# Kernel optimization log

Hardware: AMD Instinct MI355X
Metric: run time of the kernel (lower is better)

The kernel has to match this reference:

```python
import jax, jax.numpy as jnp
import numpy as np

H = 64
VOCAB = 128
LN_EPS = 1e-5
NORM_EPS = 1e-12


def _l2norm(k):
    # F.normalize(..., dim=-1): x / max(||x||_2, eps)
    n = jnp.sqrt(jnp.sum(k * k, axis=-1, keepdims=True))
    return k / jnp.maximum(n, NORM_EPS)


def _delta_scan(M0, ks, vs):
    # ks, vs: [L, B, H] time-major; M0: [B, H, H]
    def step(M, kv):
        k, v = kv
        Mk = jnp.einsum('bij,bj->bi', M, k)            # [B,H]
        M = M + (v - Mk)[:, :, None] * k[:, None, :]   # rank-1 update
        return M, None
    M, _ = jax.lax.scan(step, M0, (ks, vs))
    return M


def reference(x, embed, W1, b1, W2, b2, ln_g, ln_b, Wk, Wv, Wq, Wattn, Wout, bout):
    # Encoder: embed -> residual FF -> LayerNorm
    h = embed[x]                                        # [B,L,H]
    ff = jnp.maximum(h @ W1.T + b1, 0.0) @ W2.T + b2
    z = h + ff
    mu = jnp.mean(z, axis=-1, keepdims=True)
    var = jnp.mean((z - mu) ** 2, axis=-1, keepdims=True)
    hidden = (z - mu) / jnp.sqrt(var + LN_EPS) * ln_g + ln_b  # [B,L,H]

    B, L, _ = hidden.shape
    # First delta-rule memory write over all L steps
    ks = _l2norm(hidden @ Wk.T)                         # [B,L,H]
    vs = hidden @ Wv.T                                  # [B,L,H]
    M0 = jnp.zeros((B, H, H), dtype=hidden.dtype)
    M = _delta_scan(M0, jnp.swapaxes(ks, 0, 1), jnp.swapaxes(vs, 0, 1))

    half = L // 2
    slots = jnp.swapaxes(M, 1, 2)                       # [B,H,H] = M^T
    q = hidden[:, :half, :] @ Wattn.T                   # [B,half,H]
    # bmm(q, slots^T) = q @ M
    attn = jax.nn.softmax(jnp.einsum('bth,bhk->btk', q, M) / jnp.sqrt(jnp.asarray(H, hidden.dtype)), axis=-1)
    ctx = jnp.einsum('btk,bkh->bth', attn, slots)       # [B,half,H]

    # Second delta-rule write seeded from M
    ks2 = _l2norm(ctx @ Wk.T)
    vs2 = ctx @ Wv.T
    M2 = _delta_scan(M, jnp.swapaxes(ks2, 0, 1), jnp.swapaxes(vs2, 0, 1))

    q_last = hidden[:, -1, :] @ Wq.T                    # [B,H]
    read = jnp.einsum('bij,bj->bi', M2, q_last)         # [B,H]
    return read @ Wout.T + bout                         # [B,VOCAB]


def setup_inputs() -> dict:
    key = jax.random.key(0)
    ks = jax.random.split(key, 16)
    B, L = 64, 4096
    s = 0.05
    return {
        'x': jax.random.randint(ks[0], (B, L), 0, VOCAB),
        'embed': jax.random.normal(ks[1], (VOCAB, H), jnp.float32) * s,
        'W1': jax.random.normal(ks[2], (2 * H, H), jnp.float32) * s,
        'b1': jnp.zeros((2 * H,), jnp.float32),
        'W2': jax.random.normal(ks[3], (H, 2 * H), jnp.float32) * s,
        'b2': jnp.zeros((H,), jnp.float32),
        'ln_g': jnp.ones((H,), jnp.float32),
        'ln_b': jnp.zeros((H,), jnp.float32),
        'Wk': jax.random.normal(ks[4], (H, H), jnp.float32) * s,
        'Wv': jax.random.normal(ks[5], (H, H), jnp.float32) * s,
        'Wq': jax.random.normal(ks[6], (H, H), jnp.float32) * s,
        'Wattn': jax.random.normal(ks[7], (H, H), jnp.float32) * s,
        'Wout': jax.random.normal(ks[8], (VOCAB, H), jnp.float32) * s,
        'bout': jnp.zeros((VOCAB,), jnp.float32),
    }
```

## Files before the change

### kernel.cpp

```cpp
#include <hip/hip_runtime.h>

#define SEQL 4096
#define NB 64

__device__ __forceinline__ float dpp_xor1_add(float x) {
    int v = __builtin_amdgcn_mov_dpp(__float_as_int(x), 0xB1, 0xF, 0xF, true);
    return x + __int_as_float(v);
}
__device__ __forceinline__ float dpp_xor2_add(float x) {
    int v = __builtin_amdgcn_mov_dpp(__float_as_int(x), 0x4E, 0xF, 0xF, true);
    return x + __int_as_float(v);
}

#define FMA16(A, W, H)                                      \
    A[0]  = fmaf(W.x, H.x, A[0]);  A[1]  = fmaf(W.x, H.y, A[1]);   \
    A[2]  = fmaf(W.x, H.z, A[2]);  A[3]  = fmaf(W.x, H.w, A[3]);   \
    A[4]  = fmaf(W.y, H.x, A[4]);  A[5]  = fmaf(W.y, H.y, A[5]);   \
    A[6]  = fmaf(W.y, H.z, A[6]);  A[7]  = fmaf(W.y, H.w, A[7]);   \
    A[8]  = fmaf(W.z, H.x, A[8]);  A[9]  = fmaf(W.z, H.y, A[9]);   \
    A[10] = fmaf(W.z, H.z, A[10]); A[11] = fmaf(W.z, H.w, A[11]);  \
    A[12] = fmaf(W.w, H.x, A[12]); A[13] = fmaf(W.w, H.y, A[13]);  \
    A[14] = fmaf(W.w, H.z, A[14]); A[15] = fmaf(W.w, H.w, A[15])

__device__ __forceinline__ void proj_tile64(const float* __restrict__ sW,
                                            const float* __restrict__ sA,
                                            int jq, int tq, float* __restrict__ a)
{
#pragma unroll
    for (int u = 0; u < 16; ++u) a[u] = 0.f;
#pragma unroll 4
    for (int i = 0; i < 64; ++i) {
        float4 w  = *reinterpret_cast<const float4*>(&sW[i * 68 + jq]);
        float4 h4 = *reinterpret_cast<const float4*>(&sA[i * 68 + tq]);
        FMA16(a, w, h4);
    }
}

__device__ __forceinline__ void load_w_t(const float* __restrict__ W, int ldw, int col0,
                                         int tid, float4* __restrict__ r)
{
    const int j = tid & 63;
    const int cq0 = tid >> 6;
#pragma unroll
    for (int it = 0; it < 4; ++it)
        r[it] = *reinterpret_cast<const float4*>(&W[(size_t)j * ldw + col0 + (it * 4 + cq0) * 4]);
}
__device__ __forceinline__ void write_w_t(const float4* __restrict__ r,
                                          float* __restrict__ sWb, int tid)
{
    const int j = tid & 63;
    const int cq0 = tid >> 6;
#pragma unroll
    for (int it = 0; it < 4; ++it) {
        const int c = (it * 4 + cq0) * 4;
        sWb[(c + 0) * 68 + j] = r[it].x;
        sWb[(c + 1) * 68 + j] = r[it].y;
        sWb[(c + 2) * 68 + j] = r[it].z;
        sWb[(c + 3) * 68 + j] = r[it].w;
    }
}

__device__ __forceinline__ void stage_w_t(const float* __restrict__ W, int ldw, int col0,
                                          float* __restrict__ sWb, int tid)
{
    float4 r[4];
    load_w_t(W, ldw, col0, tid, r);
    write_w_t(r, sWb, tid);
}
__device__ __forceinline__ void stage_w_n(const float* __restrict__ W,
                                          float* __restrict__ sWb, int tid)
{
#pragma unroll
    for (int it = 0; it < 4; ++it) {
        int item = it * 256 + tid;
        int r = item >> 4, c4 = item & 15;
        float4 w = *reinterpret_cast<const float4*>(&W[(size_t)r * 64 + c4 * 4]);
        *reinterpret_cast<float4*>(&sWb[r * 68 + c4 * 4]) = w;
    }
}

__global__ __launch_bounds__(256) void encoder_kernel(
    const int* __restrict__ x, const float* __restrict__ embed,
    const float* __restrict__ W1, const float* __restrict__ b1,
    const float* __restrict__ W2, const float* __restrict__ b2,
    const float* __restrict__ ln_g, const float* __restrict__ ln_b,
    const float* __restrict__ Wk, const float* __restrict__ Wv,
    const float* __restrict__ Wq,
    float* __restrict__ ks, float* __restrict__ vs,
    float* __restrict__ hidT, float* __restrict__ qlast)
{
    __shared__ __align__(16) float sZ[64 * 68];
    __shared__ __align__(16) float sF[64 * 68];
    __shared__ __align__(16) float sW[64 * 68];

    const int tid = threadIdx.x;
    const size_t g0 = (size_t)blockIdx.x * 64;
    const int b = (int)(g0 >> 12);
    const int l0 = (int)(g0 & (SEQL - 1));
    const int jq = (tid & 15) * 4;
    const int tq = (tid >> 4) * 4;
    const bool doq = (l0 < 2048);
    const bool dolast = (l0 == SEQL - 64);

    float4 pf[4], pf2[4];

    load_w_t(W1, 64, 0, tid, pf);
    for (int idx = tid; idx < 4096; idx += 256) {
        int t = idx >> 6, i = idx & 63;
        sZ[i * 68 + t] = embed[(size_t)x[g0 + t] * 64 + i];
    }
    write_w_t(pf, sW, tid);
    load_w_t(W2, 128, 0, tid, pf2);
    __syncthreads();

    float zacc[16];
#pragma unroll
    for (int u = 0; u < 16; ++u) zacc[u] = 0.f;

    {
        float a[16];
        proj_tile64(sW, sZ, jq, tq, a);
        float4 bb = *reinterpret_cast<const float4*>(&b1[jq]);
        float bv[4] = {bb.x, bb.y, bb.z, bb.w};
#pragma unroll
        for (int u = 0; u < 4; ++u) {
            float4 o;
            o.x = fmaxf(a[u * 4 + 0] + bv[u], 0.f);
            o.y = fmaxf(a[u * 4 + 1] + bv[u], 0.f);
            o.z = fmaxf(a[u * 4 + 2] + bv[u], 0.f);
            o.w = fmaxf(a[u * 4 + 3] + bv[u], 0.f);
            *reinterpret_cast<float4*>(&sF[(jq + u) * 68 + tq]) = o;
        }
    }
    __syncthreads();
    write_w_t(pf2, sW, tid);
    load_w_t(W1 + 4096, 64, 0, tid, pf);
    __syncthreads();
#pragma unroll 4
    for (int p = 0; p < 64; ++p) {
        float4 w  = *reinterpret_cast<const float4*>(&sW[p * 68 + jq]);
        float4 f4 = *reinterpret_cast<const float4*>(&sF[p * 68 + tq]);
        FMA16(zacc, w, f4);
    }
    __syncthreads();
    write_w_t(pf, sW, tid);
    load_w_t(W2, 128, 64, tid, pf2);
    __syncthreads();
    {
        float a[16];
        proj_tile64(sW, sZ, jq, tq, a);
        float4 bb = *reinterpret_cast<const float4*>(&b1[64 + jq]);
        float bv[4] = {bb.x, bb.y, bb.z, bb.w};
#pragma unroll
        for (int u = 0; u < 4; ++u) {
            float4 o;
            o.x = fmaxf(a[u * 4 + 0] + bv[u], 0.f);
            o.y = fmaxf(a[u * 4 + 1] + bv[u], 0.f);
            o.z = fmaxf(a[u * 4 + 2] + bv[u], 0.f);
            o.w = fmaxf(a[u * 4 + 3] + bv[u], 0.f);
            *reinterpret_cast<float4*>(&sF[(jq + u) * 68 + tq]) = o;
        }
    }
    __syncthreads();
    write_w_t(pf2, sW, tid);
    load_w_t(Wk, 64, 0, tid, pf);
    load_w_t(Wv, 64, 0, tid, pf2);
    __syncthreads();
#pragma unroll 4
    for (int p = 0; p < 64; ++p) {
        float4 w  = *reinterpret_cast<const float4*>(&sW[p * 68 + jq]);
        float4 f4 = *reinterpret_cast<const float4*>(&sF[p * 68 + tq]);
        FMA16(zacc, w, f4);
    }

    {
        float z[16];
        float4 b2v = *reinterpret_cast<const float4*>(&b2[jq]);
        float bv[4] = {b2v.x, b2v.y, b2v.z, b2v.w};
#pragma unroll
        for (int u = 0; u < 4; ++u) {
            float4 h4 = *reinterpret_cast<const float4*>(&sZ[(jq + u) * 68 + tq]);
            z[u * 4 + 0] = h4.x + bv[u] + zacc[u * 4 + 0];
            z[u * 4 + 1] = h4.y + bv[u] + zacc[u * 4 + 1];
            z[u * 4 + 2] = h4.z + bv[u] + zacc[u * 4 + 2];
            z[u * 4 + 3] = h4.w + bv[u] + zacc[u * 4 + 3];
        }
        float s[4], ss[4];
#pragma unroll
        for (int v = 0; v < 4; ++v) {
            s[v]  = z[v] + z[4 + v] + z[8 + v] + z[12 + v];
            ss[v] = z[v] * z[v] + z[4 + v] * z[4 + v]
                  + z[8 + v] * z[8 + v] + z[12 + v] * z[12 + v];
        }
#pragma unroll
        for (int m = 1; m <= 8; m <<= 1) {
#pragma unroll
            for (int v = 0; v < 4; ++v) {
                s[v]  += __shfl_xor(s[v], m);
                ss[v] += __shfl_xor(ss[v], m);
            }
        }
        float mu[4], inv[4];
#pragma unroll
        for (int v = 0; v < 4; ++v) {
            mu[v] = s[v] * 0.015625f;
            float var = ss[v] * 0.015625f - mu[v] * mu[v];
            inv[v] = rsqrtf(var + 1e-5f);
        }
        float4 g4  = *reinterpret_cast<const float4*>(&ln_g[jq]);
        float4 be4 = *reinterpret_cast<const float4*>(&ln_b[jq]);
        float gv[4] = {g4.x, g4.y, g4.z, g4.w};
        float bev[4] = {be4.x, be4.y, be4.z, be4.w};
#pragma unroll
        for (int u = 0; u < 4; ++u) {
            float4 o;
            o.x = (z[u * 4 + 0] - mu[0]) * inv[0] * gv[u] + bev[u];
            o.y = (z[u * 4 + 1] - mu[1]) * inv[1] * gv[u] + bev[u];
            o.z = (z[u * 4 + 2] - mu[2]) * inv[2] * gv[u] + bev[u];
            o.w = (z[u * 4 + 3] - mu[3]) * inv[3] * gv[u] + bev[u];
            *reinterpret_cast<float4*>(&sZ[(jq + u) * 68 + tq]) = o;
        }
    }
    __syncthreads();
    write_w_t(pf, sW, tid);
    write_w_t(pf2, sF, tid);
    if (dolast) load_w_t(Wq, 64, 0, tid, pf);
    __syncthreads();

    {
        float a[16];
        proj_tile64(sW, sZ, jq, tq, a);
        float ssq[4];
#pragma unroll
        for (int v = 0; v < 4; ++v)
            ssq[v] = a[v] * a[v] + a[4 + v] * a[4 + v]
                   + a[8 + v] * a[8 + v] + a[12 + v] * a[12 + v];
#pragma unroll
        for (int m = 1; m <= 8; m <<= 1) {
#pragma unroll
            for (int v = 0; v < 4; ++v) ssq[v] += __shfl_xor(ssq[v], m);
        }
#pragma unroll
        for (int v = 0; v < 4; ++v) {
            float sc = 1.f / fmaxf(sqrtf(ssq[v]), 1e-12f);
            float4 o = make_float4(a[v] * sc, a[4 + v] * sc, a[8 + v] * sc, a[12 + v] * sc);
            *reinterpret_cast<float4*>(&ks[(g0 + tq + v) * 64 + jq]) = o;
        }
    }
    {
        float a[16];
        proj_tile64(sF, sZ, jq, tq, a);
#pragma unroll
        for (int v = 0; v < 4; ++v) {
            float4 o = make_float4(a[v], a[4 + v], a[8 + v], a[12 + v]);
            *reinterpret_cast<float4*>(&vs[(g0 + tq + v) * 64 + jq]) = o;
        }
    }

    if (doq) {
#pragma unroll
        for (int it = 0; it < 4; ++it) {
            int item = it * 256 + tid;
            int i = item >> 4, q4 = (item & 15) * 4;
            float4 v = *reinterpret_cast<const float4*>(&sZ[i * 68 + q4]);
            *reinterpret_cast<float4*>(&hidT[((size_t)b * 64 + i) * 2048 + l0 + q4]) = v;
        }
    }

    if (dolast) {
        __syncthreads();
        write_w_t(pf, sW, tid);
        __syncthreads();
        float a[16];
        proj_tile64(sW, sZ, jq, tq, a);
        if ((tid >> 4) == 15) {
            float4 o = make_float4(a[3], a[7], a[11], a[15]);
            *reinterpret_cast<float4*>(&qlast[(size_t)b * 64 + jq]) = o;
        }
    }
}

__global__ __launch_bounds__(256) void precompute_kernel(
    const float* __restrict__ Mbuf, const float* __restrict__ Wattn,
    const float* __restrict__ Wk, const float* __restrict__ Wv,
    float* __restrict__ WAM, float* __restrict__ MK, float* __restrict__ MV)
{
    __shared__ __align__(16) float sM[64 * 68];
    __shared__ __align__(16) float sOp[64 * 68];
    const int b = blockIdx.x;
    const int tid = threadIdx.x;
    const int jq = (tid & 15) * 4;
    const int tq = (tid >> 4) * 4;
    const float* Mb = Mbuf + (size_t)b * 4096;

    stage_w_n(Mb, sM, tid);
    stage_w_n(Wattn, sOp, tid);
    __syncthreads();
    {
        float a[16];
        proj_tile64(sM, sOp, jq, tq, a);
#pragma unroll
        for (int v = 0; v < 4; ++v)
            *reinterpret_cast<float4*>(&WAM[(size_t)b * 4096 + (tq + v) * 64 + jq]) =
                make_float4(a[v], a[4 + v], a[8 + v], a[12 + v]);
    }
    __syncthreads();
    stage_w_t(Wk, 64, 0, sOp, tid);
    __syncthreads();
    {
        float a[16];
        proj_tile64(sM, sOp, jq, tq, a);
#pragma unroll
        for (int v = 0; v < 4; ++v)
            *reinterpret_cast<float4*>(&MK[(size_t)b * 4096 + (tq + v) * 64 + jq]) =
                make_float4(a[v], a[4 + v], a[8 + v], a[12 + v]);
    }
    __syncthreads();
    stage_w_t(Wv, 64, 0, sOp, tid);
    __syncthreads();
    {
        float a[16];
        proj_tile64(sM, sOp, jq, tq, a);
#pragma unroll
        for (int v = 0; v < 4; ++v)
            *reinterpret_cast<float4*>(&MV[(size_t)b * 4096 + (tq + v) * 64 + jq]) =
                make_float4(a[v], a[4 + v], a[8 + v], a[12 + v]);
    }
}

#define STEP2(K0, K1, K2, K3, V)                                                \
    do {                                                                        \
        float dp0 = fmaf(p[0], K0.x, fmaf(p[1], K0.y, fmaf(p[2], K0.z, p[3] * K0.w))); \
        float dp1 = fmaf(p[4], K1.x, fmaf(p[5], K1.y, fmaf(p[6], K1.z, p[7] * K1.w))); \
        float dp2 = fmaf(p[8], K2.x, fmaf(p[9], K2.y, fmaf(p[10], K2.z, p[11] * K2.w))); \
        float dp3 = fmaf(p[12], K3.x, fmaf(p[13], K3.y, fmaf(p[14], K3.z, p[15] * K3.w))); \
        float dq0 = fmaf(q[0], K0.x, fmaf(q[1], K0.y, fmaf(q[2], K0.z, q[3] * K0.w))); \
        float dq1 = fmaf(q[4], K1.x, fmaf(q[5], K1.y, fmaf(q[6], K1.z, q[7] * K1.w))); \
        float dq2 = fmaf(q[8], K2.x, fmaf(q[9], K2.y, fmaf(q[10], K2.z, q[11] * K2.w))); \
        float dq3 = fmaf(q[12], K3.x, fmaf(q[13], K3.y, fmaf(q[14], K3.z, q[15] * K3.w))); \
        float ddp = (dp0 + dp1) + (dp2 + dp3);                                  \
        float ddq = (dq0 + dq1) + (dq2 + dq3);                                  \
        ddp = dpp_xor1_add(ddp);  ddq = dpp_xor1_add(ddq);                      \
        ddp = dpp_xor2_add(ddp);  ddq = dpp_xor2_add(ddq);                      \
        float up = -ddp;                                                        \
        float uq = V - ddq;                                                     \
        p[0] = fmaf(up, K0.x, p[0]);   q[0] = fmaf(uq, K0.x, q[0]);             \
        p[1] = fmaf(up, K0.y, p[1]);   q[1] = fmaf(uq, K0.y, q[1]);             \
        p[2] = fmaf(up, K0.z, p[2]);   q[2] = fmaf(uq, K0.z, q[2]);             \
        p[3] = fmaf(up, K0.w, p[3]);   q[3] = fmaf(uq, K0.w, q[3]);             \
        p[4] = fmaf(up, K1.x, p[4]);   q[4] = fmaf(uq, K1.x, q[4]);             \
        p[5] = fmaf(up, K1.y, p[5]);   q[5] = fmaf(uq, K1.y, q[5]);             \
        p[6] = fmaf(up, K1.z, p[6]);   q[6] = fmaf(uq, K1.z, q[6]);             \
        p[7] = fmaf(up, K1.w, p[7]);   q[7] = fmaf(uq, K1.w, q[7]);             \
        p[8] = fmaf(up, K2.x, p[8]);   q[8] = fmaf(uq, K2.x, q[8]);             \
        p[9] = fmaf(up, K2.y, p[9]);   q[9] = fmaf(uq, K2.y, q[9]);             \
        p[10] = fmaf(up, K2.z, p[10]); q[10] = fmaf(uq, K2.z, q[10]);           \
        p[11] = fmaf(up, K2.w, p[11]); q[11] = fmaf(uq, K2.w, q[11]);           \
        p[12] = fmaf(up, K3.x, p[12]); q[12] = fmaf(uq, K3.x, q[12]);           \
        p[13] = fmaf(up, K3.y, p[13]); q[13] = fmaf(uq, K3.y, q[13]);           \
        p[14] = fmaf(up, K3.z, p[14]); q[14] = fmaf(uq, K3.z, q[14]);           \
        p[15] = fmaf(up, K3.w, p[15]); q[15] = fmaf(uq, K3.w, q[15]);           \
    } while (0)

__global__ __launch_bounds__(256) void chunk_kernel(
    float* __restrict__ ksb, float* __restrict__ vsb, int C)
{
    __shared__ __align__(16) float sk[2][32 * 64];
    __shared__ __align__(16) float sv[2][32 * 64];

    const int job = blockIdx.x;
    const int tid = threadIdx.x;
    const int r = tid >> 2;
    const int c0 = (tid & 3) * 16;
    float* kc = ksb + (size_t)job * C * 64;
    float* vc = vsb + (size_t)job * C * 64;

    float p[16], q[16];
#pragma unroll
    for (int j = 0; j < 16; ++j) { p[j] = (c0 + j == r) ? 1.f : 0.f; q[j] = 0.f; }

    const int nt = C >> 5;
    float4 rk0, rk1, rv0, rv1;

    {
        const float4* gk = reinterpret_cast<const float4*>(kc);
        const float4* gv = reinterpret_cast<const float4*>(vc);
        float4 a0 = gk[tid], a1 = gk[256 + tid];
        float4 b0 = gv[tid], b1 = gv[256 + tid];
        float4* dk = reinterpret_cast<float4*>(sk[0]);
        float4* dv = reinterpret_cast<float4*>(sv[0]);
        dk[tid] = a0; dk[256 + tid] = a1;
        dv[tid] = b0; dv[256 + tid] = b1;
    }
    if (nt > 1) {
        const float4* gk = reinterpret_cast<const float4*>(kc + 2048);
        const float4* gv = reinterpret_cast<const float4*>(vc + 2048);
        rk0 = gk[tid]; rk1 = gk[256 + tid];
        rv0 = gv[tid]; rv1 = gv[256 + tid];
    }
    __syncthreads();

    int cur = 0;
    for (int tile = 0; tile < nt; ++tile) {
        if (tile + 1 < nt) {
            float4* dk = reinterpret_cast<float4*>(sk[cur ^ 1]);
            float4* dv = reinterpret_cast<float4*>(sv[cur ^ 1]);
            dk[tid] = rk0; dk[256 + tid] = rk1;
            dv[tid] = rv0; dv[256 + tid] = rv1;
            if (tile + 2 < nt) {
                const float4* gk = reinterpret_cast<const float4*>(kc + (size_t)(tile + 2) * 2048);
                const float4* gv = reinterpret_cast<const float4*>(vc + (size_t)(tile + 2) * 2048);
                rk0 = gk[tid]; rk1 = gk[256 + tid];
                rv0 = gv[tid]; rv1 = gv[256 + tid];
            }
        }

        const float* kl = sk[cur] + c0;
        const float* vl = sv[cur] + r;
        float4 a0, a1, a2, a3, e0, e1, e2, e3;
        float va, ve;
        {
            const float4* kp = reinterpret_cast<const float4*>(kl);
            a0 = kp[0]; a1 = kp[1]; a2 = kp[2]; a3 = kp[3];
            va = vl[0];
        }
#pragma unroll
        for (int t = 0; t < 32; t += 2) {
            {
                const float4* kp = reinterpret_cast<const float4*>(kl + (t + 1) * 64);
                e0 = kp[0]; e1 = kp[1]; e2 = kp[2]; e3 = kp[3];
                ve = vl[(t + 1) * 64];
            }
            STEP2(a0, a1, a2, a3, va);
            if (t + 2 < 32) {
                const float4* kp = reinterpret_cast<const float4*>(kl + (t + 2) * 64);
                a0 = kp[0]; a1 = kp[1]; a2 = kp[2]; a3 = kp[3];
                va = vl[(t + 2) * 64];
            }
            STEP2(e0, e1, e2, e3, ve);
        }
        __syncthreads();
        cur ^= 1;
    }

    float4* po = reinterpret_cast<float4*>(kc + r * 64 + c0);
    po[0] = make_float4(p[0], p[1], p[2], p[3]);
    po[1] = make_float4(p[4], p[5], p[6], p[7]);
    po[2] = make_float4(p[8], p[9], p[10], p[11]);
    po[3] = make_float4(p[12], p[13], p[14], p[15]);
    float4* qo = reinterpret_cast<float4*>(vc + r * 64 + c0);
    qo[0] = make_float4(q[0], q[1], q[2], q[3]);
    qo[1] = make_float4(q[4], q[5], q[6], q[7]);
    qo[2] = make_float4(q[8], q[9], q[10], q[11]);
    qo[3] = make_float4(q[12], q[13], q[14], q[15]);
}

__global__ __launch_bounds__(256) void combine_kernel(
    const float* __restrict__ Pb, const float* __restrict__ Qb,
    const float* __restrict__ Min, float* __restrict__ Mout,
    int nc, int chunk_stride)
{
    __shared__ __align__(16) float sP[2][64 * 64];
    __shared__ __align__(16) float sM[2][16 * 68];
    const int bb = blockIdx.x;
    const int b = bb >> 2;
    const int r0 = (bb & 3) << 4;
    const int tid = threadIdx.x;
    const int rl = tid >> 4;
    const int j4 = (tid & 15) * 4;
    const int gr = r0 + rl;

    if (Min) {
        *reinterpret_cast<float4*>(&sM[0][rl * 68 + j4]) =
            *reinterpret_cast<const float4*>(Min + ((size_t)b * 64 + gr) * 64 + j4);
    } else {
        *reinterpret_cast<float4*>(&sM[0][rl * 68 + j4]) = make_float4(0.f, 0.f, 0.f, 0.f);
    }
    {
        const float4* g = reinterpret_cast<const float4*>(Pb + (size_t)b * nc * chunk_stride);
        float4* s = reinterpret_cast<float4*>(sP[0]);
        for (int i = tid; i < 1024; i += 256) s[i] = g[i];
    }
    __syncthreads();

    int cur = 0;
    for (int c = 0; c < nc; ++c) {
        const size_t cbase = (size_t)(b * nc + c) * chunk_stride;
        float4 rp0, rp1, rp2, rp3;
        if (c + 1 < nc) {
            const float4* g = reinterpret_cast<const float4*>(Pb + cbase + chunk_stride);
            rp0 = g[tid]; rp1 = g[tid + 256]; rp2 = g[tid + 512]; rp3 = g[tid + 768];
        }
        float4 rq = *reinterpret_cast<const float4*>(Qb + cbase + (size_t)gr * 64 + j4);

        float ax = 0.f, ay = 0.f, az = 0.f, aw = 0.f;
        const float* Mrow = &sM[cur][rl * 68];
        const float* Pl = sP[c & 1];
#pragma unroll 4
        for (int mg = 0; mg < 16; ++mg) {
            float4 a4 = *reinterpret_cast<const float4*>(Mrow + mg * 4);
            float4 p0 = *reinterpret_cast<const float4*>(Pl + (mg * 4 + 0) * 64 + j4);
            float4 p1 = *reinterpret_cast<const float4*>(Pl + (mg * 4 + 1) * 64 + j4);
            float4 p2 = *reinterpret_cast<const float4*>(Pl + (mg * 4 + 2) * 64 + j4);
            float4 p3 = *reinterpret_cast<const float4*>(Pl + (mg * 4 + 3) * 64 + j4);
            ax = fmaf(a4.x, p0.x, ax); ay = fmaf(a4.x, p0.y, ay);
            az = fmaf(a4.x, p0.z, az); aw = fmaf(a4.x, p0.w, aw);
            ax = fmaf(a4.y, p1.x, ax); ay = fmaf(a4.y, p1.y, ay);
            az = fmaf(a4.y, p1.z, az); aw = fmaf(a4.y, p1.w, aw);
            ax = fmaf(a4.z, p2.x, ax); ay = fmaf(a4.z, p2.y, ay);
            az = fmaf(a4.z, p2.z, az); aw = fmaf(a4.z, p2.w, aw);
            ax = fmaf(a4.w, p3.x, ax); ay = fmaf(a4.w, p3.y, ay);
            az = fmaf(a4.w, p3.z, az); aw = fmaf(a4.w, p3.w, aw);
        }
        const int nxt = cur ^ 1;
        *reinterpret_cast<float4*>(&sM[nxt][rl * 68 + j4]) =
            make_float4(ax + rq.x, ay + rq.y, az + rq.z, aw + rq.w);
        if (c + 1 < nc) {
            float4* s = reinterpret_cast<float4*>(sP[(c + 1) & 1]);
            s[tid] = rp0; s[tid + 256] = rp1; s[tid + 512] = rp2; s[tid + 768] = rp3;
        }
        __syncthreads();
        cur = nxt;
    }
    *reinterpret_cast<float4*>(Mout + ((size_t)b * 64 + gr) * 64 + j4) =
        *reinterpret_cast<const float4*>(&sM[cur][rl * 68 + j4]);
}

__global__ __launch_bounds__(256) void attn_kernel(
    const float* __restrict__ hidT, const float* __restrict__ WAM,
    const float* __restrict__ MK, const float* __restrict__ MV,
    float* __restrict__ ks2, float* __restrict__ vs2)
{
    __shared__ __align__(16) float sW1[64 * 68];
    __shared__ __align__(16) float sW2[64 * 68];
    __shared__ __align__(16) float sA[64 * 68];

    const int b = blockIdx.y;
    const int tile0 = blockIdx.x * 64;
    const int tid = threadIdx.x;
    const int jq = (tid & 15) * 4;
    const int tq = (tid >> 4) * 4;
    const size_t qbase = (size_t)b * 2048 + tile0;
    const float* hb = hidT + (size_t)b * 64 * 2048 + tile0;

    float4 pfk[4];
    stage_w_n(WAM + (size_t)b * 4096, sW1, tid);
    stage_w_t(MV + (size_t)b * 4096, 64, 0, sW2, tid);
#pragma unroll
    for (int it = 0; it < 4; ++it) {
        int item = it * 256 + tid;
        int i = item >> 4, q4 = (item & 15) * 4;
        float4 v = *reinterpret_cast<const float4*>(&hb[(size_t)i * 2048 + q4]);
        *reinterpret_cast<float4*>(&sA[i * 68 + q4]) = v;
    }
    load_w_t(MK + (size_t)b * 4096, 64, 0, tid, pfk);
    __syncthreads();

    float a[16];
    proj_tile64(sW1, sA, jq, tq, a);
#pragma unroll
    for (int u = 0; u < 16; ++u) a[u] *= 0.125f;

    {
        float mx[4], sm[4];
#pragma unroll
        for (int v = 0; v < 4; ++v)
            mx[v] = fmaxf(fmaxf(a[v], a[4 + v]), fmaxf(a[8 + v], a[12 + v]));
#pragma unroll
        for (int m = 1; m <= 8; m <<= 1) {
#pragma unroll
            for (int v = 0; v < 4; ++v) mx[v] = fmaxf(mx[v], __shfl_xor(mx[v], m));
        }
#pragma unroll
        for (int v = 0; v < 4; ++v) {
            a[v]      = __expf(a[v]      - mx[v]);
            a[4 + v]  = __expf(a[4 + v]  - mx[v]);
            a[8 + v]  = __expf(a[8 + v]  - mx[v]);
            a[12 + v] = __expf(a[12 + v] - mx[v]);
            sm[v] = a[v] + a[4 + v] + a[8 + v] + a[12 + v];
        }
#pragma unroll
        for (int m = 1; m <= 8; m <<= 1) {
#pragma unroll
            for (int v = 0; v < 4; ++v) sm[v] += __shfl_xor(sm[v], m);
        }
        float rinv[4];
#pragma unroll
        for (int v = 0; v < 4; ++v) rinv[v] = 1.f / sm[v];
#pragma unroll
        for (int v = 0; v < 4; ++v) {
            a[v] *= rinv[v]; a[4 + v] *= rinv[v];
            a[8 + v] *= rinv[v]; a[12 + v] *= rinv[v];
        }
    }
    __syncthreads();
#pragma unroll
    for (int u = 0; u < 4; ++u)
        *reinterpret_cast<float4*>(&sA[(jq + u) * 68 + tq]) =
            make_float4(a[u * 4 + 0], a[u * 4 + 1], a[u * 4 + 2], a[u * 4 + 3]);
    write_w_t(pfk, sW1, tid);
    __syncthreads();

    float ak[16], av[16];
#pragma unroll
    for (int u = 0; u < 16; ++u) { ak[u] = 0.f; av[u] = 0.f; }
#pragma unroll 2
    for (int i = 0; i < 64; ++i) {
        float4 wk = *reinterpret_cast<const float4*>(&sW1[i * 68 + jq]);
        float4 wv = *reinterpret_cast<const float4*>(&sW2[i * 68 + jq]);
        float4 p4 = *reinterpret_cast<const float4*>(&sA[i * 68 + tq]);
        FMA16(ak, wk, p4);
        FMA16(av, wv, p4);
    }

    {
        float ssq[4];
#pragma unroll
        for (int v = 0; v < 4; ++v)
            ssq[v] = ak[v] * ak[v] + ak[4 + v] * ak[4 + v]
                   + ak[8 + v] * ak[8 + v] + ak[12 + v] * ak[12 + v];
#pragma unroll
        for (int m = 1; m <= 8; m <<= 1) {
#pragma unroll
            for (int v = 0; v < 4; ++v) ssq[v] += __shfl_xor(ssq[v], m);
        }
#pragma unroll
        for (int v = 0; v < 4; ++v) {
            float sc = 1.f / fmaxf(sqrtf(ssq[v]), 1e-12f);
            const size_t o = (qbase + tq + v) * 64 + jq;
            *reinterpret_cast<float4*>(&ks2[o]) =
                make_float4(ak[v] * sc, ak[4 + v] * sc, ak[8 + v] * sc, ak[12 + v] * sc);
            *reinterpret_cast<float4*>(&vs2[o]) =
                make_float4(av[v], av[4 + v], av[8 + v], av[12 + v]);
        }
    }
}

__global__ __launch_bounds__(256) void final_kernel(
    const float* __restrict__ Pb, const float* __restrict__ Qb,
    const float* __restrict__ Mbuf, const float* __restrict__ qlast,
    const float* __restrict__ Wout, const float* __restrict__ bout,
    float* __restrict__ out, int nc, int chunk_stride)
{
    __shared__ float s[64], qv[64], rv[64];
    const int b = blockIdx.x;
    const int tid = threadIdx.x;
    const int r = tid >> 2;
    const int c0 = (tid & 3) * 16;

    if (tid < 64) { s[tid] = qlast[(size_t)b * 64 + tid]; qv[tid] = 0.f; }
    __syncthreads();

    for (int c = nc - 1; c >= 0; --c) {
        const size_t base = (size_t)(b * nc + c) * chunk_stride + (size_t)r * 64 + c0;
        const float4* gp = reinterpret_cast<const float4*>(Pb + base);
        const float4* gq = reinterpret_cast<const float4*>(Qb + base);
        float4 P0 = gp[0], P1 = gp[1], P2 = gp[2], P3 = gp[3];
        float4 Q0 = gq[0], Q1 = gq[1], Q2 = gq[2], Q3 = gq[3];
        const float4* sv4 = reinterpret_cast<const float4*>(&s[c0]);
        float4 s0 = sv4[0], s1 = sv4[1], s2 = sv4[2], s3 = sv4[3];

        float dp = 0.f, dq = 0.f;
        dp = fmaf(P0.x, s0.x, dp); dp = fmaf(P0.y, s0.y, dp);
        dp = fmaf(P0.z, s0.z, dp); dp = fmaf(P0.w, s0.w, dp);
        dp = fmaf(P1.x, s1.x, dp); dp = fmaf(P1.y, s1.y, dp);
        dp = fmaf(P1.z, s1.z, dp); dp = fmaf(P1.w, s1.w, dp);
        dp = fmaf(P2.x, s2.x, dp); dp = fmaf(P2.y, s2.y, dp);
        dp = fmaf(P2.z, s2.z, dp); dp = fmaf(P2.w, s2.w, dp);
        dp = fmaf(P3.x, s3.x, dp); dp = fmaf(P3.y, s3.y, dp);
        dp = fmaf(P3.z, s3.z, dp); dp = fmaf(P3.w, s3.w, dp);
        dq = fmaf(Q0.x, s0.x, dq); dq = fmaf(Q0.y, s0.y, dq);
        dq = fmaf(Q0.z, s0.z, dq); dq = fmaf(Q0.w, s0.w, dq);
        dq = fmaf(Q1.x, s1.x, dq); dq = fmaf(Q1.y, s1.y, dq);
        dq = fmaf(Q1.z, s1.z, dq); dq = fmaf(Q1.w, s1.w, dq);
        dq = fmaf(Q2.x, s2.x, dq); dq = fmaf(Q2.y, s2.y, dq);
        dq = fmaf(Q2.z, s2.z, dq); dq = fmaf(Q2.w, s2.w, dq);
        dq = fmaf(Q3.x, s3.x, dq); dq = fmaf(Q3.y, s3.y, dq);
        dq = fmaf(Q3.z, s3.z, dq); dq = fmaf(Q3.w, s3.w, dq);
        dp = dpp_xor1_add(dp); dp = dpp_xor2_add(dp);
        dq = dpp_xor1_add(dq); dq = dpp_xor2_add(dq);

        __syncthreads();
        if ((tid & 3) == 0) { s[r] = dp; qv[r] += dq; }
        __syncthreads();
    }

    {
        const float4* gm = reinterpret_cast<const float4*>(
            Mbuf + (size_t)b * 4096 + (size_t)r * 64 + c0);
        float4 M0 = gm[0], M1 = gm[1], M2v = gm[2], M3 = gm[3];
        const float4* sv4 = reinterpret_cast<const float4*>(&s[c0]);
        float4 s0 = sv4[0], s1 = sv4[1], s2 = sv4[2], s3 = sv4[3];
        float d = 0.f;
        d = fmaf(M0.x, s0.x, d); d = fmaf(M0.y, s0.y, d);
        d = fmaf(M0.z, s0.z, d); d = fmaf(M0.w, s0.w, d);
        d = fmaf(M1.x, s1.x, d); d = fmaf(M1.y, s1.y, d);
        d = fmaf(M1.z, s1.z, d); d = fmaf(M1.w, s1.w, d);
        d = fmaf(M2v.x, s2.x, d); d = fmaf(M2v.y, s2.y, d);
        d = fmaf(M2v.z, s2.z, d); d = fmaf(M2v.w, s2.w, d);
        d = fmaf(M3.x, s3.x, d); d = fmaf(M3.y, s3.y, d);
        d = fmaf(M3.z, s3.z, d); d = fmaf(M3.w, s3.w, d);
        d = dpp_xor1_add(d); d = dpp_xor2_add(d);
        if ((tid & 3) == 0) rv[r] = d + qv[r];
    }
    __syncthreads();

    if (tid < 128) {
        const float* wr = Wout + (size_t)tid * 64;
        float a0 = 0.f, a1 = 0.f, a2 = 0.f, a3 = 0.f;
#pragma unroll
        for (int h = 0; h < 64; h += 4) {
            a0 = fmaf(wr[h],     rv[h],     a0);
            a1 = fmaf(wr[h + 1], rv[h + 1], a1);
            a2 = fmaf(wr[h + 2], rv[h + 2], a2);
            a3 = fmaf(wr[h + 3], rv[h + 3], a3);
        }
        out[(size_t)b * 128 + tid] = bout[tid] + (a0 + a1) + (a2 + a3);
    }
}

extern "C" void kernel_launch(void* const* d_in, const int* in_sizes, int n_in,
                              void* d_out, int out_size, void* d_ws, size_t ws_size,
                              hipStream_t stream)
{
    const int* x        = (const int*)d_in[0];
    const float* embed  = (const float*)d_in[1];
    const float* W1     = (const float*)d_in[2];
    const float* b1     = (const float*)d_in[3];
    const float* W2     = (const float*)d_in[4];
    const float* b2     = (const float*)d_in[5];
    const float* ln_g   = (const float*)d_in[6];
    const float* ln_b   = (const float*)d_in[7];
    const float* Wk     = (const float*)d_in[8];
    const float* Wv     = (const float*)d_in[9];
    const float* Wq     = (const float*)d_in[10];
    const float* Wattn  = (const float*)d_in[11];
    const float* Wout   = (const float*)d_in[12];
    const float* bout   = (const float*)d_in[13];

    float* ws = (float*)d_ws;
    float* ks  = ws;
    float* vs  = ks  + (size_t)NB * SEQL * 64;
    float* hid = vs  + (size_t)NB * SEQL * 64;
    float* ql  = hid + (size_t)NB * 2048 * 64;
    float* M   = ql  + (size_t)NB * 64;
    float* WAM = M   + (size_t)NB * 64 * 64;
    float* MK  = WAM + (size_t)NB * 64 * 64;
    float* MV  = MK  + (size_t)NB * 64 * 64;
    if (ws_size < (size_t)(MV + (size_t)NB * 64 * 64 - ws) * sizeof(float)) return;

    hipLaunchKernelGGL(encoder_kernel, dim3((NB * SEQL) / 64), dim3(256), 0, stream,
                       x, embed, W1, b1, W2, b2, ln_g, ln_b, Wk, Wv, Wq,
                       ks, vs, hid, ql);

    const int C1 = 256, nc1 = SEQL / C1;
    hipLaunchKernelGGL(chunk_kernel, dim3(NB * nc1), dim3(256), 0, stream, ks, vs, C1);
    hipLaunchKernelGGL(combine_kernel, dim3(NB * 4), dim3(256), 0, stream,
                       ks, vs, (const float*)nullptr, M, nc1, C1 * 64);

    hipLaunchKernelGGL(precompute_kernel, dim3(NB), dim3(256), 0, stream,
                       M, Wattn, Wk, Wv, WAM, MK, MV);

    hipLaunchKernelGGL(attn_kernel, dim3(32, NB), dim3(256), 0, stream,
                       hid, WAM, MK, MV, ks, vs);

    const int C2 = 128, nc2 = 2048 / C2;
    hipLaunchKernelGGL(chunk_kernel, dim3(NB * nc2), dim3(256), 0, stream, ks, vs, C2);
    hipLaunchKernelGGL(final_kernel, dim3(NB), dim3(256), 0, stream,
                       ks, vs, M, ql, Wout, bout, (float*)d_out, nc2, C2 * 64);
}
```

Measured before the change: 467.6 us.

## Fuse precompute into combine kernel via last-block atomic counter

Removes the separate precompute kernel launch. Each batch's four combine blocks increment an atomic counter, and the last one to finish computes M·Wattn, M·Wk and M·Wv for that batch. The counter is reset inside chunk_kernel. This saves one kernel launch and its serialization gap, but adds threadfences, an atomic and a serial tail on 64 blocks.

```diff
diff --git a/kernel.cpp b/kernel.cpp
--- a/kernel.cpp
+++ b/kernel.cpp
@@ -277,54 +277,6 @@
             float4 o = make_float4(a[3], a[7], a[11], a[15]);
             *reinterpret_cast<float4*>(&qlast[(size_t)b * 64 + jq]) = o;
         }
-    }
-}
-
-__global__ __launch_bounds__(256) void precompute_kernel(
-    const float* __restrict__ Mbuf, const float* __restrict__ Wattn,
-    const float* __restrict__ Wk, const float* __restrict__ Wv,
-    float* __restrict__ WAM, float* __restrict__ MK, float* __restrict__ MV)
-{
-    __shared__ __align__(16) float sM[64 * 68];
-    __shared__ __align__(16) float sOp[64 * 68];
-    const int b = blockIdx.x;
-    const int tid = threadIdx.x;
-    const int jq = (tid & 15) * 4;
-    const int tq = (tid >> 4) * 4;
-    const float* Mb = Mbuf + (size_t)b * 4096;
-
-    stage_w_n(Mb, sM, tid);
-    stage_w_n(Wattn, sOp, tid);
-    __syncthreads();
-    {
-        float a[16];
-        proj_tile64(sM, sOp, jq, tq, a);
-#pragma unroll
-        for (int v = 0; v < 4; ++v)
-            *reinterpret_cast<float4*>(&WAM[(size_t)b * 4096 + (tq + v) * 64 + jq]) =
-                make_float4(a[v], a[4 + v], a[8 + v], a[12 + v]);
-    }
-    __syncthreads();
-    stage_w_t(Wk, 64, 0, sOp, tid);
-    __syncthreads();
-    {
-        float a[16];
-        proj_tile64(sM, sOp, jq, tq, a);
-#pragma unroll
-        for (int v = 0; v < 4; ++v)
-            *reinterpret_cast<float4*>(&MK[(size_t)b * 4096 + (tq + v) * 64 + jq]) =
-                make_float4(a[v], a[4 + v], a[8 + v], a[12 + v]);
-    }
-    __syncthreads();
-    stage_w_t(Wv, 64, 0, sOp, tid);
-    __syncthreads();
-    {
-        float a[16];
-        proj_tile64(sM, sOp, jq, tq, a);
-#pragma unroll
-        for (int v = 0; v < 4; ++v)
-            *reinterpret_cast<float4*>(&MV[(size_t)b * 4096 + (tq + v) * 64 + jq]) =
-                make_float4(a[v], a[4 + v], a[8 + v], a[12 + v]);
     }
 }
 
@@ -363,7 +315,7 @@
     } while (0)
 
 __global__ __launch_bounds__(256) void chunk_kernel(
-    float* __restrict__ ksb, float* __restrict__ vsb, int C)
+    float* __restrict__ ksb, float* __restrict__ vsb, int C, int* __restrict__ cnt)
 {
     __shared__ __align__(16) float sk[2][32 * 64];
     __shared__ __align__(16) float sv[2][32 * 64];
@@ -374,6 +326,8 @@
     const int c0 = (tid & 3) * 16;
     float* kc = ksb + (size_t)job * C * 64;
     float* vc = vsb + (size_t)job * C * 64;
+
+    if (tid == 0 && job < NB) cnt[job] = 0;
 
     float p[16], q[16];
 #pragma unroll
@@ -457,11 +411,17 @@
 
 __global__ __launch_bounds__(256) void combine_kernel(
     const float* __restrict__ Pb, const float* __restrict__ Qb,
-    const float* __restrict__ Min, float* __restrict__ Mout,
-    int nc, int chunk_stride)
-{
-    __shared__ __align__(16) float sP[2][64 * 64];
-    __shared__ __align__(16) float sM[2][16 * 68];
+    float* __restrict__ Mout, int nc, int chunk_stride,
+    const float* __restrict__ Wattn, const float* __restrict__ Wk,
+    const float* __restrict__ Wv,
+    float* __restrict__ WAM, float* __restrict__ MK, float* __restrict__ MV,
+    int* __restrict__ cnt)
+{
+    __shared__ __align__(16) float lds[10368];
+    __shared__ int sWin;
+    float* sP  = lds;
+    float* sMl = lds + 8192;
+
     const int bb = blockIdx.x;
     const int b = bb >> 2;
     const int r0 = (bb & 3) << 4;
@@ -470,15 +430,10 @@
     const int j4 = (tid & 15) * 4;
     const int gr = r0 + rl;
 
-    if (Min) {
-        *reinterpret_cast<float4*>(&sM[0][rl * 68 + j4]) =
-            *reinterpret_cast<const float4*>(Min + ((size_t)b * 64 + gr) * 64 + j4);
-    } else {
-        *reinterpret_cast<float4*>(&sM[0][rl * 68 + j4]) = make_float4(0.f, 0.f, 0.f, 0.f);
-    }
+    *reinterpret_cast<float4*>(&sMl[rl * 68 + j4]) = make_float4(0.f, 0.f, 0.f, 0.f);
     {
         const float4* g = reinterpret_cast<const float4*>(Pb + (size_t)b * nc * chunk_stride);
-        float4* s = reinterpret_cast<float4*>(sP[0]);
+        float4* s = reinterpret_cast<float4*>(sP);
         for (int i = tid; i < 1024; i += 256) s[i] = g[i];
     }
     __syncthreads();
@@ -494,8 +449,8 @@
         float4 rq = *reinterpret_cast<const float4*>(Qb + cbase + (size_t)gr * 64 + j4);
 
         float ax = 0.f, ay = 0.f, az = 0.f, aw = 0.f;
-        const float* Mrow = &sM[cur][rl * 68];
-        const float* Pl = sP[c & 1];
+        const float* Mrow = &sMl[cur * 1088 + rl * 68];
+        const float* Pl = sP + (c & 1) * 4096;
 #pragma unroll 4
         for (int mg = 0; mg < 16; ++mg) {
             float4 a4 = *reinterpret_cast<const float4*>(Mrow + mg * 4);
@@ -513,17 +468,68 @@
             az = fmaf(a4.w, p3.z, az); aw = fmaf(a4.w, p3.w, aw);
         }
         const int nxt = cur ^ 1;
-        *reinterpret_cast<float4*>(&sM[nxt][rl * 68 + j4]) =
+        *reinterpret_cast<float4*>(&sMl[nxt * 1088 + rl * 68 + j4]) =
             make_float4(ax + rq.x, ay + rq.y, az + rq.z, aw + rq.w);
         if (c + 1 < nc) {
-            float4* s = reinterpret_cast<float4*>(sP[(c + 1) & 1]);
+            float4* s = reinterpret_cast<float4*>(sP + ((c + 1) & 1) * 4096);
             s[tid] = rp0; s[tid + 256] = rp1; s[tid + 512] = rp2; s[tid + 768] = rp3;
         }
         __syncthreads();
         cur = nxt;
     }
     *reinterpret_cast<float4*>(Mout + ((size_t)b * 64 + gr) * 64 + j4) =
-        *reinterpret_cast<const float4*>(&sM[cur][rl * 68 + j4]);
+        *reinterpret_cast<const float4*>(&sMl[cur * 1088 + rl * 68 + j4]);
+
+    __threadfence();
+    __syncthreads();
+    if (tid == 0) {
+        int old = atomicAdd(&cnt[b], 1);
+        sWin = (old == 3) ? 1 : 0;
+    }
+    __syncthreads();
+    if (!sWin) return;
+    __threadfence();
+
+    float* pcM  = lds;
+    float* pcOp = lds + 4352;
+    const int jq = (tid & 15) * 4;
+    const int tq = (tid >> 4) * 4;
+    const float* Mb = Mout + (size_t)b * 4096;
+
+    __syncthreads();
+    stage_w_n(Mb, pcM, tid);
+    stage_w_n(Wattn, pcOp, tid);
+    __syncthreads();
+    {
+        float a[16];
+        proj_tile64(pcM, pcOp, jq, tq, a);
+#pragma unroll
+        for (int v = 0; v < 4; ++v)
+            *reinterpret_cast<float4*>(&WAM[(size_t)b * 4096 + (tq + v) * 64 + jq]) =
+                make_float4(a[v], a[4 + v], a[8 + v], a[12 + v]);
+    }
+    __syncthreads();
+    stage_w_t(Wk, 64, 0, pcOp, tid);
+    __syncthreads();
+    {
+        float a[16];
+        proj_tile64(pcM, pcOp, jq, tq, a);
+#pragma unroll
+        for (int v = 0; v < 4; ++v)
+            *reinterpret_cast<float4*>(&MK[(size_t)b * 4096 + (tq + v) * 64 + jq]) =
+                make_float4(a[v], a[4 + v], a[8 + v], a[12 + v]);
+    }
+    __syncthreads();
+    stage_w_t(Wv, 64, 0, pcOp, tid);
+    __syncthreads();
+    {
+        float a[16];
+        proj_tile64(pcM, pcOp, jq, tq, a);
+#pragma unroll
+        for (int v = 0; v < 4; ++v)
+            *reinterpret_cast<float4*>(&MV[(size_t)b * 4096 + (tq + v) * 64 + jq]) =
+                make_float4(a[v], a[4 + v], a[8 + v], a[12 + v]);
+    }
 }
 
 __global__ __launch_bounds__(256) void attn_kernel(
@@ -747,25 +753,24 @@
     float* WAM = M   + (size_t)NB * 64 * 64;
     float* MK  = WAM + (size_t)NB * 64 * 64;
     float* MV  = MK  + (size_t)NB * 64 * 64;
-    if (ws_size < (size_t)(MV + (size_t)NB * 64 * 64 - ws) * sizeof(float)) return;
+    int*   cnt = (int*)(MV + (size_t)NB * 64 * 64);
+    if (ws_size < ((size_t)(MV + (size_t)NB * 64 * 64 - ws) + NB) * sizeof(float)) return;
 
     hipLaunchKernelGGL(encoder_kernel, dim3((NB * SEQL) / 64), dim3(256), 0, stream,
                        x, embed, W1, b1, W2, b2, ln_g, ln_b, Wk, Wv, Wq,
                        ks, vs, hid, ql);
 
     const int C1 = 256, nc1 = SEQL / C1;
-    hipLaunchKernelGGL(chunk_kernel, dim3(NB * nc1), dim3(256), 0, stream, ks, vs, C1);
+    hipLaunchKernelGGL(chunk_kernel, dim3(NB * nc1), dim3(256), 0, stream, ks, vs, C1, cnt);
     hipLaunchKernelGGL(combine_kernel, dim3(NB * 4), dim3(256), 0, stream,
-                       ks, vs, (const float*)nullptr, M, nc1, C1 * 64);
-
-    hipLaunchKernelGGL(precompute_kernel, dim3(NB), dim3(256), 0, stream,
-                       M, Wattn, Wk, Wv, WAM, MK, MV);
+                       ks, vs, M, nc1, C1 * 64,
+                       Wattn, Wk, Wv, WAM, MK, MV, cnt);
 
     hipLaunchKernelGGL(attn_kernel, dim3(32, NB), dim3(256), 0, stream,
                        hid, WAM, MK, MV, ks, vs);
 
     const int C2 = 128, nc2 = 2048 / C2;
-    hipLaunchKernelGGL(chunk_kernel, dim3(NB * nc2), dim3(256), 0, stream, ks, vs, C2);
+    hipLaunchKernelGGL(chunk_kernel, dim3(NB * nc2), dim3(256), 0, stream, ks, vs, C2, cnt);
     hipLaunchKernelGGL(final_kernel, dim3(NB), dim3(256), 0, stream,
                        ks, vs, M, ql, Wout, bout, (float*)d_out, nc2, C2 * 64);
 }
```

New measurement: 501.7 us. +7.3%, slower.
